# Optimization experiments

Measured on AMD Instinct MI355X. Metric: run time of the kernel, lower is better.

## Reference

```python
import jax, jax.numpy as jnp
import numpy as np


def setup_inputs() -> dict:
    key = jax.random.key(0)
    ks = jax.random.split(key, 9)
    C_in, C_out, D = 64, 64, 24
    B, H, W = 4, 96, 96
    s_in = 1.0 / np.sqrt(C_in)
    s_d = 1.0 / np.sqrt(D)
    return {
        "x": jax.random.normal(ks[0], (B, C_in, H, W), dtype=jnp.float32),
        "wq": jax.random.uniform(ks[1], (D, C_in), jnp.float32, -s_in, s_in),
        "bq": jax.random.uniform(ks[2], (D,), jnp.float32, -s_in, s_in),
        "wk": jax.random.uniform(ks[3], (D, C_in), jnp.float32, -s_in, s_in),
        "bk": jax.random.uniform(ks[4], (D,), jnp.float32, -s_in, s_in),
        "wv": jax.random.uniform(ks[5], (D, C_in), jnp.float32, -s_in, s_in),
        "bv": jax.random.uniform(ks[6], (D,), jnp.float32, -s_in, s_in),
        "wo": jax.random.uniform(ks[7], (C_out, D), jnp.float32, -s_d, s_d),
        "bo": jax.random.uniform(ks[8], (C_out,), jnp.float32, -s_d, s_d),
    }


def reference(x, wq, bq, wk, bk, wv, bv, wo, bo):
    B, C, H, W = x.shape
    D = wq.shape[0]
    xf = x.reshape(B, C, H * W)  # [B, C, N]
    # 1x1 convs == channel-wise linear projections
    q = jnp.einsum('dc,bcn->bdn', wq, xf) + bq[None, :, None]  # [B, D, N]
    k = jnp.einsum('dc,bcn->bdn', wk, xf) + bk[None, :, None]
    v = jnp.einsum('dc,bcn->bdn', wv, xf) + bv[None, :, None]
    scale = 1.0 / jnp.sqrt(jnp.asarray(D, x.dtype))
    scores = jnp.einsum('bdi,bdj->bij', q, k) * scale  # [B, N, N]
    weights = jax.nn.softmax(scores, axis=-1)
    # attn_out[b,d,i] = sum_j v[b,d,j] * weights[b,i,j]
    attn = jnp.einsum('bdj,bij->bdi', v, weights)  # [B, D, N]
    out = jnp.einsum('od,bdn->bon', wo, attn) + bo[None, :, None]
    return out.reshape(B, -1, H, W)
```

## Files before the change

kernel.cpp:

```cpp
#include <hip/hip_runtime.h>
#include <stdint.h>

#define NPIX 9216
#define CIN 64
#define DD 24
#define DP 32
#define JQ 2304
#define NIT 36

typedef __attribute__((ext_vector_type(8))) short short8;
typedef __attribute__((ext_vector_type(4))) float f32x4;
typedef __attribute__((ext_vector_type(4))) unsigned int u32x4;

__device__ __forceinline__ unsigned short f2bf(float f) {
    unsigned int u = __builtin_bit_cast(unsigned int, f);
    u += 0x7fffu + ((u >> 16) & 1u);
    return (unsigned short)(u >> 16);
}
__device__ __forceinline__ unsigned int pkbf(float lo, float hi) {
    unsigned int r;
    asm("v_cvt_pk_bf16_f32 %0, %1, %2" : "=v"(r) : "v"(lo), "v"(hi));
    return r;
}

__global__ __launch_bounds__(256) void qkv_proj_kernel(
    const float* __restrict__ x,
    const float* __restrict__ wq, const float* __restrict__ bq,
    const float* __restrict__ wk, const float* __restrict__ bk,
    const float* __restrict__ wv, const float* __restrict__ bv,
    unsigned short* __restrict__ qr, unsigned short* __restrict__ kr,
    unsigned short* __restrict__ vdn)
{
    const int p = blockIdx.y;
    const int tid = blockIdx.x * 256 + threadIdx.x;
    const int b = tid / NPIX;
    const int n = tid - b * NPIX;
    const float* xb = x + (size_t)b * CIN * NPIX + n;
    float xv[CIN];
#pragma unroll
    for (int c = 0; c < CIN; ++c) xv[c] = xb[(size_t)c * NPIX];

    const float* wm = (p == 0) ? wq : (p == 1) ? wk : wv;
    const float* bm = (p == 0) ? bq : (p == 1) ? bk : bv;

    float acc[DD];
#pragma unroll
    for (int d = 0; d < DD; ++d) acc[d] = bm[d];
#pragma unroll 4
    for (int c = 0; c < CIN; ++c) {
        const float xc = xv[c];
#pragma unroll
        for (int d = 0; d < DD; ++d) acc[d] = fmaf(wm[d * CIN + c], xc, acc[d]);
    }

    if (p == 2) {
        const size_t vbase = (size_t)b * DD * NPIX + n;
#pragma unroll
        for (int d = 0; d < DD; ++d) vdn[vbase + (size_t)d * NPIX] = f2bf(acc[d]);
    } else {
        alignas(16) unsigned short row[DP];
        const float sc = (p == 0) ? (float)(0.20412414523193154 * 1.4426950408889634) : 1.0f;
#pragma unroll
        for (int d = 0; d < DD; ++d) row[d] = f2bf(acc[d] * sc);
#pragma unroll
        for (int d = DD; d < DP; ++d) row[d] = 0;
        unsigned short* dst = ((p == 0) ? qr : kr) + (size_t)(b * NPIX + n) * DP;
        const u32x4* r4 = (const u32x4*)row;
#pragma unroll
        for (int i = 0; i < 4; ++i) ((u32x4*)dst)[i] = r4[i];
    }
}

__global__ __launch_bounds__(512) void attn_kernel(
    const unsigned short* __restrict__ qr,
    const unsigned short* __restrict__ kr,
    const unsigned short* __restrict__ vdn,
    const float* __restrict__ wo, const float* __restrict__ bo,
    float* __restrict__ out)
{
    __shared__ __align__(16) unsigned char pool[20480 + 18432];
    __shared__ float wo_lds[64 * DD];
    __shared__ float bo_lds[64];
    unsigned short* kpool = (unsigned short*)pool;
    unsigned short* vpool = (unsigned short*)(pool + 20480);

    const int b = blockIdx.y, tile = blockIdx.x;
    const int t = threadIdx.x;
    const int w = t >> 6, lane = t & 63;
    const int g = lane >> 4, c = lane & 15;
    const int sq = w >> 2;
    const int p  = w & 3;

    for (int i = t; i < 64 * DD; i += 512) wo_lds[i] = wo[i];
    if (t < 64) bo_lds[t] = bo[t];

    for (int i = t; i < 4 * 8 * 72; i += 512) {
        const int q_ = i / 576, rem = i - q_ * 576;
        const int r_ = rem / 72, col = rem - r_ * 72;
        vpool[q_ * 2304 + (24 + r_) * 72 + col] = (r_ == 0) ? (unsigned short)0x3F80 : 0;
    }

    const int qbaseA = tile * 64 + sq * 32 + c;
    const short8 qfA = *(const short8*)(qr + ((size_t)(b * NPIX + qbaseA)) * DP + g * 8);
    const short8 qfB = *(const short8*)(qr + ((size_t)(b * NPIX + qbaseA + 16)) * DP + g * 8);

    const unsigned short* kb = kr + (size_t)b * NPIX * DP;
    const unsigned short* vb = vdn + (size_t)b * DD * NPIX;

    const int khw = t & 1, kq = t >> 7, kjn = (t >> 1) & 63;
    const int kR = ((kjn >> 5) & 1) * 32 + ((kjn >> 2) & 1) * 16
                 + ((kjn >> 4) & 1) * 8 + ((kjn >> 3) & 1) * 4 + (kjn & 3);
    unsigned short* kdst = kpool + kq * 2560 + kR * 40 + khw * 16;
    const unsigned short* ksrc0 = kb + ((size_t)(kq * JQ + kjn)) * DP + khw * 16;

    const int vq = t / 96, vrem = t - vq * 96, vd = vrem >> 2, vpt = t & 3;
    unsigned short* vdst = vpool + vq * 2304 + vd * 72 + vpt * 16;
    const unsigned short* vsrc0 = vb + (size_t)vd * NPIX + vq * JQ + vpt * 16;

    const unsigned short* kT = kpool + p * 2560;
    const unsigned short* vT = vpool + p * 2304;

    f32x4 aA0 = {0.f, 0.f, 0.f, 0.f};
    f32x4 aA1 = {0.f, 0.f, 0.f, 0.f};
    f32x4 aB0 = {0.f, 0.f, 0.f, 0.f};
    f32x4 aB1 = {0.f, 0.f, 0.f, 0.f};
    const f32x4 zf = {0.f, 0.f, 0.f, 0.f};

    u32x4 pk0, pk1, pv0, pv1;
    {
        const u32x4* sk = (const u32x4*)ksrc0;
        pk0 = sk[0]; pk1 = sk[1];
        if (t < 384) { const u32x4* sv = (const u32x4*)vsrc0; pv0 = sv[0]; pv1 = sv[1]; }
    }

    for (int it = 0; it < NIT; ++it) {
        __syncthreads();
        *(u32x4*)kdst = pk0; *(u32x4*)(kdst + 8) = pk1;
        if (t < 384) { *(u32x4*)vdst = pv0; *(u32x4*)(vdst + 8) = pv1; }
        __syncthreads();

        if (it + 1 < NIT) {
            const int jn = (it + 1) * 64;
            const u32x4* sk = (const u32x4*)(ksrc0 + (size_t)jn * DP);
            pk0 = sk[0]; pk1 = sk[1];
            if (t < 384) { const u32x4* sv = (const u32x4*)(vsrc0 + jn); pv0 = sv[0]; pv1 = sv[1]; }
        }

        const short8 kf0 = *(const short8*)(kT + ( 0 + c) * 40 + g * 8);
        const short8 kf1 = *(const short8*)(kT + (16 + c) * 40 + g * 8);
        const short8 kf2 = *(const short8*)(kT + (32 + c) * 40 + g * 8);
        const short8 kf3 = *(const short8*)(kT + (48 + c) * 40 + g * 8);
        __builtin_amdgcn_s_setprio(1);
        f32x4 sA0 = __builtin_amdgcn_mfma_f32_16x16x32_bf16(kf0, qfA, zf, 0, 0, 0);
        f32x4 sA1 = __builtin_amdgcn_mfma_f32_16x16x32_bf16(kf1, qfA, zf, 0, 0, 0);
        f32x4 sA2 = __builtin_amdgcn_mfma_f32_16x16x32_bf16(kf2, qfA, zf, 0, 0, 0);
        f32x4 sA3 = __builtin_amdgcn_mfma_f32_16x16x32_bf16(kf3, qfA, zf, 0, 0, 0);
        f32x4 sB0 = __builtin_amdgcn_mfma_f32_16x16x32_bf16(kf0, qfB, zf, 0, 0, 0);
        f32x4 sB1 = __builtin_amdgcn_mfma_f32_16x16x32_bf16(kf1, qfB, zf, 0, 0, 0);
        f32x4 sB2 = __builtin_amdgcn_mfma_f32_16x16x32_bf16(kf2, qfB, zf, 0, 0, 0);
        f32x4 sB3 = __builtin_amdgcn_mfma_f32_16x16x32_bf16(kf3, qfB, zf, 0, 0, 0);
        __builtin_amdgcn_s_setprio(0);

        union { short8 s8; unsigned int u32[4]; } fa0, fa1, fb0, fb1;
        {
            float p0[4], p1[4], p2[4], p3[4];
#pragma unroll
            for (int r = 0; r < 4; ++r) {
                p0[r] = __builtin_amdgcn_exp2f(sA0[r]);
                p1[r] = __builtin_amdgcn_exp2f(sA1[r]);
                p2[r] = __builtin_amdgcn_exp2f(sA2[r]);
                p3[r] = __builtin_amdgcn_exp2f(sA3[r]);
            }
            fa0.u32[0] = pkbf(p0[0], p0[1]); fa0.u32[1] = pkbf(p0[2], p0[3]);
            fa0.u32[2] = pkbf(p1[0], p1[1]); fa0.u32[3] = pkbf(p1[2], p1[3]);
            fa1.u32[0] = pkbf(p2[0], p2[1]); fa1.u32[1] = pkbf(p2[2], p2[3]);
            fa1.u32[2] = pkbf(p3[0], p3[1]); fa1.u32[3] = pkbf(p3[2], p3[3]);
        }
        {
            float p0[4], p1[4], p2[4], p3[4];
#pragma unroll
            for (int r = 0; r < 4; ++r) {
                p0[r] = __builtin_amdgcn_exp2f(sB0[r]);
                p1[r] = __builtin_amdgcn_exp2f(sB1[r]);
                p2[r] = __builtin_amdgcn_exp2f(sB2[r]);
                p3[r] = __builtin_amdgcn_exp2f(sB3[r]);
            }
            fb0.u32[0] = pkbf(p0[0], p0[1]); fb0.u32[1] = pkbf(p0[2], p0[3]);
            fb0.u32[2] = pkbf(p1[0], p1[1]); fb0.u32[3] = pkbf(p1[2], p1[3]);
            fb1.u32[0] = pkbf(p2[0], p2[1]); fb1.u32[1] = pkbf(p2[2], p2[3]);
            fb1.u32[2] = pkbf(p3[0], p3[1]); fb1.u32[3] = pkbf(p3[2], p3[3]);
        }

        const short8 vl0 = *(const short8*)(vT + (c)      * 72 +      g * 8);
        const short8 vh0 = *(const short8*)(vT + (16 + c) * 72 +      g * 8);
        const short8 vl1 = *(const short8*)(vT + (c)      * 72 + 32 + g * 8);
        const short8 vh1 = *(const short8*)(vT + (16 + c) * 72 + 32 + g * 8);
        __builtin_amdgcn_s_setprio(1);
        aA0 = __builtin_amdgcn_mfma_f32_16x16x32_bf16(vl0, fa0.s8, aA0, 0, 0, 0);
        aA1 = __builtin_amdgcn_mfma_f32_16x16x32_bf16(vh0, fa0.s8, aA1, 0, 0, 0);
        aA0 = __builtin_amdgcn_mfma_f32_16x16x32_bf16(vl1, fa1.s8, aA0, 0, 0, 0);
        aA1 = __builtin_amdgcn_mfma_f32_16x16x32_bf16(vh1, fa1.s8, aA1, 0, 0, 0);
        aB0 = __builtin_amdgcn_mfma_f32_16x16x32_bf16(vl0, fb0.s8, aB0, 0, 0, 0);
        aB1 = __builtin_amdgcn_mfma_f32_16x16x32_bf16(vh0, fb0.s8, aB1, 0, 0, 0);
        aB0 = __builtin_amdgcn_mfma_f32_16x16x32_bf16(vl1, fb1.s8, aB0, 0, 0, 0);
        aB1 = __builtin_amdgcn_mfma_f32_16x16x32_bf16(vh1, fb1.s8, aB1, 0, 0, 0);
        __builtin_amdgcn_s_setprio(0);
    }
    __syncthreads();

    float* om = (float*)pool;
    *(f32x4*)(om + (w * 32 + c) * 36 + 4 * g) = aA0;
    *(f32x4*)(om + (w * 32 + c) * 36 + 16 + 4 * g) = aA1;
    *(f32x4*)(om + (w * 32 + 16 + c) * 36 + 4 * g) = aB0;
    *(f32x4*)(om + (w * 32 + 16 + c) * 36 + 16 + 4 * g) = aB1;
    __syncthreads();

    const int q = t & 63, og = t >> 6;
    const int sqe = q >> 5, qc = q & 31;
    const float* o0 = om + ((sqe * 4 + 0) * 32 + qc) * 36;
    const float* o1 = om + ((sqe * 4 + 1) * 32 + qc) * 36;
    const float* o2 = om + ((sqe * 4 + 2) * 32 + qc) * 36;
    const float* o3 = om + ((sqe * 4 + 3) * 32 + qc) * 36;
    const float inv = 1.0f / (o0[24] + o1[24] + o2[24] + o3[24]);
    float od[DD];
#pragma unroll
    for (int d = 0; d < DD; ++d)
        od[d] = (o0[d] + o1[d] + o2[d] + o3[d]) * inv;

    const int n_g = tile * 64 + q;
#pragma unroll
    for (int oo = 0; oo < 8; ++oo) {
        const int o = og * 8 + oo;
        float a = bo_lds[o];
#pragma unroll
        for (int d = 0; d < DD; ++d) a = fmaf(wo_lds[o * DD + d], od[d], a);
        out[((size_t)(b * 64 + o)) * NPIX + n_g] = a;
    }
}

extern "C" void kernel_launch(void* const* d_in, const int* in_sizes, int n_in,
                              void* d_out, int out_size, void* d_ws, size_t ws_size,
                              hipStream_t stream) {
    const float* x  = (const float*)d_in[0];
    const float* wq = (const float*)d_in[1];
    const float* bq = (const float*)d_in[2];
    const float* wk = (const float*)d_in[3];
    const float* bk = (const float*)d_in[4];
    const float* wv = (const float*)d_in[5];
    const float* bv = (const float*)d_in[6];
    const float* wo = (const float*)d_in[7];
    const float* bo = (const float*)d_in[8];
    float* out = (float*)d_out;

    unsigned short* qr  = (unsigned short*)d_ws;
    unsigned short* kr  = qr + (size_t)4 * NPIX * DP;
    unsigned short* vdn = kr + (size_t)4 * NPIX * DP;

    hipLaunchKernelGGL(qkv_proj_kernel, dim3(4 * NPIX / 256, 3), dim3(256), 0, stream,
                       x, wq, bq, wk, bk, wv, bv, qr, kr, vdn);
    hipLaunchKernelGGL(attn_kernel, dim3(NPIX / 64, 4), dim3(512), 0, stream,
                       qr, kr, vdn, wo, bo, out);
}
```

Measured before the change: 102.3 us.

## Split attention over two key halves and add a separate combine kernel

The attention kernel now splits the key/value range into two halves via a new grid dimension, which doubles the block count. Each block writes un-normalized partial numerators and the softmax denominator to workspace instead of finishing the output. A new combine kernel sums the two partials, normalizes, and applies the output projection. The aim is better CU load balance and less tail imbalance with only 576 large blocks. The cost is an extra launch, partial-sum traffic through global memory, and repeating the Q load and per-block setup in each half.

```diff
diff --git a/kernel.cpp b/kernel.cpp
--- a/kernel.cpp
+++ b/kernel.cpp
@@ -5,8 +5,8 @@
 #define CIN 64
 #define DD 24
 #define DP 32
-#define JQ 2304
-#define NIT 36
+#define JQ 1152
+#define NIT 18
 
 typedef __attribute__((ext_vector_type(8))) short short8;
 typedef __attribute__((ext_vector_type(4))) float f32x4;
@@ -75,25 +75,19 @@
     const unsigned short* __restrict__ qr,
     const unsigned short* __restrict__ kr,
     const unsigned short* __restrict__ vdn,
-    const float* __restrict__ wo, const float* __restrict__ bo,
-    float* __restrict__ out)
+    float* __restrict__ part)
 {
     __shared__ __align__(16) unsigned char pool[20480 + 18432];
-    __shared__ float wo_lds[64 * DD];
-    __shared__ float bo_lds[64];
     unsigned short* kpool = (unsigned short*)pool;
     unsigned short* vpool = (unsigned short*)(pool + 20480);
 
-    const int b = blockIdx.y, tile = blockIdx.x;
+    const int tile = blockIdx.x, jh = blockIdx.y, b = blockIdx.z;
     const int t = threadIdx.x;
     const int w = t >> 6, lane = t & 63;
     const int g = lane >> 4, c = lane & 15;
     const int sq = w >> 2;
     const int p  = w & 3;
 
-    for (int i = t; i < 64 * DD; i += 512) wo_lds[i] = wo[i];
-    if (t < 64) bo_lds[t] = bo[t];
-
     for (int i = t; i < 4 * 8 * 72; i += 512) {
         const int q_ = i / 576, rem = i - q_ * 576;
         const int r_ = rem / 72, col = rem - r_ * 72;
@@ -106,16 +100,17 @@
 
     const unsigned short* kb = kr + (size_t)b * NPIX * DP;
     const unsigned short* vb = vdn + (size_t)b * DD * NPIX;
+    const int jbase = jh * 4608;
 
     const int khw = t & 1, kq = t >> 7, kjn = (t >> 1) & 63;
     const int kR = ((kjn >> 5) & 1) * 32 + ((kjn >> 2) & 1) * 16
                  + ((kjn >> 4) & 1) * 8 + ((kjn >> 3) & 1) * 4 + (kjn & 3);
     unsigned short* kdst = kpool + kq * 2560 + kR * 40 + khw * 16;
-    const unsigned short* ksrc0 = kb + ((size_t)(kq * JQ + kjn)) * DP + khw * 16;
+    const unsigned short* ksrc0 = kb + ((size_t)(jbase + kq * JQ + kjn)) * DP + khw * 16;
 
     const int vq = t / 96, vrem = t - vq * 96, vd = vrem >> 2, vpt = t & 3;
     unsigned short* vdst = vpool + vq * 2304 + vd * 72 + vpt * 16;
-    const unsigned short* vsrc0 = vb + (size_t)vd * NPIX + vq * JQ + vpt * 16;
+    const unsigned short* vsrc0 = vb + (size_t)vd * NPIX + jbase + vq * JQ + vpt * 16;
 
     const unsigned short* kT = kpool + p * 2560;
     const unsigned short* vT = vpool + p * 2304;
@@ -221,16 +216,49 @@
     const float* o1 = om + ((sqe * 4 + 1) * 32 + qc) * 36;
     const float* o2 = om + ((sqe * 4 + 2) * 32 + qc) * 36;
     const float* o3 = om + ((sqe * 4 + 3) * 32 + qc) * 36;
-    const float inv = 1.0f / (o0[24] + o1[24] + o2[24] + o3[24]);
+    float* dst = part + ((size_t)((b * 2 + jh) * NPIX + tile * 64 + q)) * 26;
+#pragma unroll
+    for (int i = 0; i < 3; ++i) {
+        const int d = og * 3 + i;
+        dst[d] = o0[d] + o1[d] + o2[d] + o3[d];
+    }
+    if (og == 7) dst[24] = o0[24] + o1[24] + o2[24] + o3[24];
+}
+
+__global__ __launch_bounds__(256) void combine_kernel(
+    const float* __restrict__ part,
+    const float* __restrict__ wo, const float* __restrict__ bo,
+    float* __restrict__ out)
+{
+    __shared__ float od_lds[64][25];
+    __shared__ float wo_lds[64 * DD];
+    __shared__ float bo_lds[64];
+    const int tile = blockIdx.x, b = blockIdx.y;
+    const int t = threadIdx.x;
+    for (int i = t; i < 64 * DD; i += 256) wo_lds[i] = wo[i];
+    if (t < 64) bo_lds[t] = bo[t];
+
+    const int q = t & 63, c2 = t >> 6;
+    {
+        const float* pA = part + ((size_t)((b * 2 + 0) * NPIX + tile * 64 + q)) * 26;
+        const float* pB = part + ((size_t)((b * 2 + 1) * NPIX + tile * 64 + q)) * 26;
+#pragma unroll
+        for (int k = 0; k < 7; ++k) {
+            const int i = c2 * 7 + k;
+            if (i < 25) od_lds[q][i] = pA[i] + pB[i];
+        }
+    }
+    __syncthreads();
+
+    const float inv = 1.0f / od_lds[q][24];
     float od[DD];
 #pragma unroll
-    for (int d = 0; d < DD; ++d)
-        od[d] = (o0[d] + o1[d] + o2[d] + o3[d]) * inv;
+    for (int d = 0; d < DD; ++d) od[d] = od_lds[q][d] * inv;
 
     const int n_g = tile * 64 + q;
 #pragma unroll
-    for (int oo = 0; oo < 8; ++oo) {
-        const int o = og * 8 + oo;
+    for (int oo = 0; oo < 16; ++oo) {
+        const int o = c2 * 16 + oo;
         float a = bo_lds[o];
 #pragma unroll
         for (int d = 0; d < DD; ++d) a = fmaf(wo_lds[o * DD + d], od[d], a);
@@ -255,9 +283,11 @@
     unsigned short* qr  = (unsigned short*)d_ws;
     unsigned short* kr  = qr + (size_t)4 * NPIX * DP;
     unsigned short* vdn = kr + (size_t)4 * NPIX * DP;
-
+    float* part = (float*)((char*)d_ws + 6488064);
     hipLaunchKernelGGL(qkv_proj_kernel, dim3(4 * NPIX / 256, 3), dim3(256), 0, stream,
                        x, wq, bq, wk, bk, wv, bv, qr, kr, vdn);
-    hipLaunchKernelGGL(attn_kernel, dim3(NPIX / 64, 4), dim3(512), 0, stream,
-                       qr, kr, vdn, wo, bo, out);
-}
+    hipLaunchKernelGGL(attn_kernel, dim3(NPIX / 64, 2, 4), dim3(512), 0, stream,
+                       qr, kr, vdn, part);
+    hipLaunchKernelGGL(combine_kernel, dim3(NPIX / 64, 4), dim3(256), 0, stream,
+                       part, wo, bo, out);
+}
```

After: 97.32 us (median of 2 runs). 4.9% less time.
